# Optimization experiments

Measured on AMD Instinct MI355X. Metric: run time of the kernel, lower is better.

## Reference

```python
import jax, jax.numpy as jnp
import numpy as np

M = 2048          # num_anchors
K = 32            # neighbors_per_anchor
RADIUS = 0.2      # search_radius
EPS = 1e-5        # BatchNorm eps


def _fps(coords, m):
    """Furthest point sampling. coords: [B,N,3] -> idx [B,m] (starts at index 0, as in torch FPS)."""
    B, N, _ = coords.shape

    def step(carry, _):
        dmin, last = carry
        pt = jnp.take_along_axis(coords, last[:, None, None], axis=1)          # [B,1,3]
        d = jnp.sum((coords - pt) ** 2, axis=-1)                                # [B,N]
        dmin = jnp.minimum(dmin, d)
        nxt = jnp.argmax(dmin, axis=-1).astype(jnp.int32)
        return (dmin, nxt), last

    dmin0 = jnp.full((B, N), 1e10, coords.dtype)
    last0 = jnp.zeros((B,), jnp.int32)
    _, idx = jax.lax.scan(step, (dmin0, last0), None, length=m)                 # [m,B]
    return jnp.transpose(idx)                                                   # [B,m]


def _ball_query(radius, k, coords, anchors):
    """First-k points within radius of each anchor; pad with first hit (PointNet++ semantics)."""
    B, N, _ = coords.shape
    d2 = jnp.sum((anchors[:, :, None, :] - coords[:, None, :, :]) ** 2, axis=-1)  # [B,M,N]
    ar = jnp.arange(N, dtype=jnp.int32)
    masked = jnp.where(d2 < radius * radius, ar[None, None, :], N)               # invalid -> N
    neg_top, _ = jax.lax.top_k(-masked, k)                                       # k smallest indices
    nb = -neg_top                                                                # [B,M,K] ascending
    first = nb[..., :1]                                                          # anchor itself always hits
    return jnp.where(nb == N, first, nb)


def _mlp_layer(x, W, g, b):
    """1x1 conv (no bias) + BatchNorm (training-mode batch stats, biased var) + ReLU.
    x: [B,M,K,Cin], W: [Cout,Cin] -> [B,M,K,Cout]."""
    y = jnp.einsum('bmkc,oc->bmko', x, W)
    mu = y.mean(axis=(0, 1, 2))
    var = y.var(axis=(0, 1, 2))
    y = (y - mu) * jax.lax.rsqrt(var + EPS) * g + b
    return jax.nn.relu(y)


def setup_inputs() -> dict:
    key = jax.random.key(0)
    ks = jax.random.split(key, 6)
    B, N, D = 4, 8192, 16
    dims = [D + 3, 64, 64, 128]
    coords = jax.random.uniform(ks[0], (B, N, 3), dtype=jnp.float32)
    features = jax.random.normal(ks[1], (B, N, D), dtype=jnp.float32)
    inp = {'coords': coords, 'features': features}
    for i in range(3):
        inp[f'W{i}'] = jax.random.normal(ks[2 + i], (dims[i + 1], dims[i]), dtype=jnp.float32) * 0.05
        inp[f'g{i}'] = jnp.ones((dims[i + 1],), jnp.float32)
        inp[f'b{i}'] = jnp.zeros((dims[i + 1],), jnp.float32)
    return inp


def reference(coords, features, W0, g0, b0, W1, g1, b1, W2, g2, b2):
    B = coords.shape[0]
    aidx = _fps(coords, M)                                                       # [B,M]
    anchors = jnp.take_along_axis(coords, aidx[..., None], axis=1)               # [B,M,3]
    nb = _ball_query(RADIUS, K, coords, anchors)                                 # [B,M,K]
    bidx = jnp.arange(B)[:, None, None]
    grouped_xyz = coords[bidx, nb] - anchors[:, :, None, :]                      # [B,M,K,3]
    grouped_feats = features[bidx, nb]                                           # [B,M,K,D]
    x = jnp.concatenate([grouped_xyz, grouped_feats], axis=-1)                   # [B,M,K,3+D]
    x = _mlp_layer(x, W0, g0, b0)
    x = _mlp_layer(x, W1, g1, b1)
    x = _mlp_layer(x, W2, g2, b2)
    aggregated = jnp.transpose(x.max(axis=2), (0, 2, 1))                         # [B,C,M]
    return anchors, aggregated
```

## Files before the change

### kernel.cpp

```cpp
#include <hip/hip_runtime.h>

#define BB 4
#define NN 8192
#define MM 2048
#define KK 32
#define RROWS (BB*MM*KK)

__device__ __forceinline__ float dist2(float ax,float ay,float az,float bx,float by,float bz){
    float dx=__fsub_rn(ax,bx), dy=__fsub_rn(ay,by), dz=__fsub_rn(az,bz);
    return __fadd_rn(__fadd_rn(__fmul_rn(dx,dx),__fmul_rn(dy,dy)),__fmul_rn(dz,dz));
}

__global__ __launch_bounds__(512, 2) void fps_kernel(const float* __restrict__ coords,
                                                     float* __restrict__ anchors)
{
    const int b = blockIdx.x, tid = threadIdx.x;
    const float* cb = coords + (size_t)b*NN*3;
    float* ab = anchors + (size_t)b*MM*3;
    float px[16],py[16],pz[16],dmin[16];
#pragma unroll
    for(int j=0;j<16;++j){
        int idx = j*512 + tid;
        px[j]=cb[idx*3+0]; py[j]=cb[idx*3+1]; pz[j]=cb[idx*3+2];
        dmin[j]=1e10f;
    }
    __shared__ unsigned long long slot[2][8];
    const int w = tid>>6;
    float lx=cb[0], ly=cb[1], lz=cb[2];
    if(tid==0){ ab[0]=lx; ab[1]=ly; ab[2]=lz; }
    for(int s=1;s<MM;++s){
        float bv=-1.f; int bi=0;
#pragma unroll
        for(int j=0;j<16;++j){
            float d = dist2(px[j],py[j],pz[j],lx,ly,lz);
            dmin[j]=fminf(dmin[j],d);
            if(dmin[j]>bv){ bv=dmin[j]; bi=j*512+tid; }
        }
        unsigned long long p = ((unsigned long long)__float_as_uint(bv)<<32) | (unsigned)(NN-1-bi);
#pragma unroll
        for(int off=32;off;off>>=1){
            unsigned long long q = __shfl_xor(p, off);
            if(q>p) p=q;
        }
        const int par = s&1;
        if((tid&63)==0) slot[par][w]=p;
        __syncthreads();
        unsigned long long p0=slot[par][0], p1=slot[par][1], p2=slot[par][2], p3=slot[par][3];
        unsigned long long p4=slot[par][4], p5=slot[par][5], p6=slot[par][6], p7=slot[par][7];
        if(p1>p0) p0=p1;
        if(p3>p2) p2=p3;
        if(p5>p4) p4=p5;
        if(p7>p6) p6=p7;
        if(p2>p0) p0=p2;
        if(p6>p4) p4=p6;
        if(p4>p0) p0=p4;
        const int win = NN-1-(int)(unsigned)p0;
        lx=cb[win*3+0]; ly=cb[win*3+1]; lz=cb[win*3+2];
        if(tid==0){ ab[s*3+0]=lx; ab[s*3+1]=ly; ab[s*3+2]=lz; }
    }
}

__global__ __launch_bounds__(256) void ballq_kernel(const float* __restrict__ coords,
                                                    const float* __restrict__ anchors,
                                                    int* __restrict__ nb)
{
    const int wid = threadIdx.x>>6, lane = threadIdx.x&63;
    const int a = blockIdx.x*4 + wid;
    const int b = a >> 11;
    const float* cb = coords + (size_t)b*NN*3;
    const float ax=anchors[a*3+0], ay=anchors[a*3+1], az=anchors[a*3+2];
    const float R2 = (float)(0.2*0.2);
    int* out = nb + (size_t)a*KK;
    int cnt = 0, first = 0;
    for(int base=0; base<NN; base+=64){
        int i = base + lane;
        float d2 = dist2(ax,ay,az, cb[i*3+0],cb[i*3+1],cb[i*3+2]);
        bool in = d2 < R2;
        unsigned long long mask = __ballot(in);
        if(cnt==0 && mask) first = base + (int)__builtin_ctzll(mask);
        int pre = __popcll(mask & ((1ull<<lane)-1ull));
        if(in && (cnt+pre)<KK) out[cnt+pre] = i;
        cnt += __popcll(mask);
        if(cnt>=KK) break;
    }
    if(cnt<KK && lane>=cnt && lane<KK) out[lane] = first;
}

__global__ __launch_bounds__(256) void l0_stats_kernel(
    const float* __restrict__ coords, const float* __restrict__ feats,
    const float* __restrict__ anchors, const int* __restrict__ nb,
    const float* __restrict__ W0, float* __restrict__ stats)
{
    const int r = blockIdx.x*256 + threadIdx.x;
    const int b = r>>16, mk = r&65535, m = mk>>5;
    const int p = nb[r];
    const float* pc = coords + ((size_t)b*NN + p)*3;
    const float* pa = anchors + ((size_t)b*MM + m)*3;
    const float* pf = feats + ((size_t)b*NN + p)*16;
    float x[19];
    x[0]=pc[0]-pa[0]; x[1]=pc[1]-pa[1]; x[2]=pc[2]-pa[2];
#pragma unroll
    for(int c=0;c<16;++c) x[3+c]=pf[c];
    __shared__ float lsum[4][64], lsq[4][64];
    const int lane = threadIdx.x&63, wid = threadIdx.x>>6;
    for(int o=0;o<64;++o){
        const float* w = W0 + o*19;
        float acc=0.f;
#pragma unroll
        for(int c=0;c<19;++c) acc = fmaf(x[c], w[c], acc);
        float s1=acc, s2=acc*acc;
#pragma unroll
        for(int off=32;off>0;off>>=1){ s1+=__shfl_xor(s1,off); s2+=__shfl_xor(s2,off); }
        if(lane==0){ lsum[wid][o]=s1; lsq[wid][o]=s2; }
    }
    __syncthreads();
    if(threadIdx.x<64){
        int o=threadIdx.x;
        atomicAdd(&stats[o],    lsum[0][o]+lsum[1][o]+lsum[2][o]+lsum[3][o]);
        atomicAdd(&stats[64+o], lsq[0][o]+lsq[1][o]+lsq[2][o]+lsq[3][o]);
    }
}

__global__ void fin_kernel(const float* __restrict__ acc, const float* __restrict__ g,
                           const float* __restrict__ bias, float* __restrict__ s,
                           float* __restrict__ sh, int C)
{
    int o = threadIdx.x; if(o>=C) return;
    const float R = (float)RROWS;
    float mu = acc[o]/R;
    float var = acc[C+o]/R - mu*mu;
    if(var<0.f) var=0.f;
    float sc = g[o] * (1.0f/sqrtf(var+1e-5f));
    s[o]=sc; sh[o]=bias[o]-mu*sc;
}

__global__ __launch_bounds__(256) void l1_kernel(
    const float* __restrict__ coords, const float* __restrict__ feats,
    const float* __restrict__ anchors, const int* __restrict__ nb,
    const float* __restrict__ W0, const float* __restrict__ W1,
    const float* __restrict__ s0, const float* __restrict__ sh0,
    float* __restrict__ y1, float* __restrict__ stats)
{
    const int r = blockIdx.x*256 + threadIdx.x;
    const int b = r>>16, mk = r&65535, m = mk>>5;
    const int p = nb[r];
    const float* pc = coords + ((size_t)b*NN + p)*3;
    const float* pa = anchors + ((size_t)b*MM + m)*3;
    const float* pf = feats + ((size_t)b*NN + p)*16;
    float x[19];
    x[0]=pc[0]-pa[0]; x[1]=pc[1]-pa[1]; x[2]=pc[2]-pa[2];
#pragma unroll
    for(int c=0;c<16;++c) x[3+c]=pf[c];
    float x1[64];
#pragma unroll
    for(int o=0;o<64;++o){
        const float* w = W0 + o*19;
        float acc=0.f;
#pragma unroll
        for(int c=0;c<19;++c) acc = fmaf(x[c], w[c], acc);
        x1[o] = fmaxf(fmaf(acc, s0[o], sh0[o]), 0.f);
    }
    __shared__ float lsum[4][64], lsq[4][64];
    const int lane = threadIdx.x&63, wid = threadIdx.x>>6;
    for(int o=0;o<64;++o){
        const float* w = W1 + o*64;
        float acc=0.f;
#pragma unroll
        for(int c=0;c<64;++c) acc = fmaf(x1[c], w[c], acc);
        y1[(size_t)o*RROWS + r] = acc;
        float s1=acc, s2=acc*acc;
#pragma unroll
        for(int off=32;off>0;off>>=1){ s1+=__shfl_xor(s1,off); s2+=__shfl_xor(s2,off); }
        if(lane==0){ lsum[wid][o]=s1; lsq[wid][o]=s2; }
    }
    __syncthreads();
    if(threadIdx.x<64){
        int o=threadIdx.x;
        atomicAdd(&stats[128+o], lsum[0][o]+lsum[1][o]+lsum[2][o]+lsum[3][o]);
        atomicAdd(&stats[192+o], lsq[0][o]+lsq[1][o]+lsq[2][o]+lsq[3][o]);
    }
}

__global__ __launch_bounds__(256) void l2_kernel(
    const float* __restrict__ y1, const float* __restrict__ W2,
    const float* __restrict__ s1, const float* __restrict__ sh1,
    float* __restrict__ maxv, float* __restrict__ minv, float* __restrict__ stats)
{
    const int r = blockIdx.x*256 + threadIdx.x;
    float x1[64];
#pragma unroll
    for(int c=0;c<64;++c)
        x1[c] = fmaxf(fmaf(y1[(size_t)c*RROWS + r], s1[c], sh1[c]), 0.f);
    __shared__ float lsum[4][128], lsq[4][128];
    const int lane = threadIdx.x&63, wid = threadIdx.x>>6;
    const size_t g = (size_t)(r>>5);
    for(int o=0;o<128;++o){
        const float* w = W2 + o*64;
        float acc=0.f;
#pragma unroll
        for(int c=0;c<64;++c) acc = fmaf(x1[c], w[c], acc);
        float mx=acc, mn=acc;
#pragma unroll
        for(int off=16;off>0;off>>=1){ mx=fmaxf(mx,__shfl_xor(mx,off)); mn=fminf(mn,__shfl_xor(mn,off)); }
        float s1v=acc, s2v=acc*acc;
#pragma unroll
        for(int off=32;off>0;off>>=1){ s1v+=__shfl_xor(s1v,off); s2v+=__shfl_xor(s2v,off); }
        if((lane&31)==0){ maxv[g*128+o]=mx; minv[g*128+o]=mn; }
        if(lane==0){ lsum[wid][o]=s1v; lsq[wid][o]=s2v; }
    }
    __syncthreads();
    if(threadIdx.x<128){
        int o=threadIdx.x;
        atomicAdd(&stats[256+o], lsum[0][o]+lsum[1][o]+lsum[2][o]+lsum[3][o]);
        atomicAdd(&stats[384+o], lsq[0][o]+lsq[1][o]+lsq[2][o]+lsq[3][o]);
    }
}

__global__ __launch_bounds__(128) void out_kernel(
    const float* __restrict__ maxv, const float* __restrict__ minv,
    const float* __restrict__ s2, const float* __restrict__ sh2,
    float* __restrict__ agg)
{
    const int gg = blockIdx.x;
    const int o = threadIdx.x;
    float s = s2[o], sh = sh2[o];
    float pick = (s >= 0.f) ? maxv[(size_t)gg*128+o] : minv[(size_t)gg*128+o];
    float v = fmaxf(fmaf(pick, s, sh), 0.f);
    const int b = gg>>11, m = gg&2047;
    agg[((size_t)b*128 + o)*MM + m] = v;
}

extern "C" void kernel_launch(void* const* d_in, const int* in_sizes, int n_in,
                              void* d_out, int out_size, void* d_ws, size_t ws_size,
                              hipStream_t stream) {
    (void)in_sizes; (void)n_in; (void)out_size; (void)ws_size;
    const float* coords = (const float*)d_in[0];
    const float* feats  = (const float*)d_in[1];
    const float* W0 = (const float*)d_in[2];
    const float* g0 = (const float*)d_in[3];
    const float* b0 = (const float*)d_in[4];
    const float* W1 = (const float*)d_in[5];
    const float* g1 = (const float*)d_in[6];
    const float* b1 = (const float*)d_in[7];
    const float* W2 = (const float*)d_in[8];
    const float* g2 = (const float*)d_in[9];
    const float* b2 = (const float*)d_in[10];

    float* out = (float*)d_out;
    float* anchors = out;
    float* agg = out + (size_t)BB*MM*3;

    char* ws = (char*)d_ws;
    int*   nb    = (int*)ws;
    float* y1v   = (float*)(ws + 1048576);
    float* maxv  = (float*)(ws + 1048576 + 67108864);
    float* minv  = maxv + (size_t)BB*MM*128;
    float* stats = minv + (size_t)BB*MM*128;
    float* s0 = stats + 512; float* sh0 = s0 + 64;
    float* s1 = sh0 + 64;    float* sh1 = s1 + 64;
    float* s2 = sh1 + 64;    float* sh2 = s2 + 128;

    hipMemsetAsync(stats, 0, 512*sizeof(float), stream);
    fps_kernel  <<<BB, 512, 0, stream>>>(coords, anchors);
    ballq_kernel<<<BB*MM/4, 256, 0, stream>>>(coords, anchors, nb);
    l0_stats_kernel<<<RROWS/256, 256, 0, stream>>>(coords, feats, anchors, nb, W0, stats);
    fin_kernel  <<<1, 64, 0, stream>>>(stats, g0, b0, s0, sh0, 64);
    l1_kernel   <<<RROWS/256, 256, 0, stream>>>(coords, feats, anchors, nb, W0, W1, s0, sh0, y1v, stats);
    fin_kernel  <<<1, 64, 0, stream>>>(stats+128, g1, b1, s1, sh1, 64);
    l2_kernel   <<<RROWS/256, 256, 0, stream>>>(y1v, W2, s1, sh1, maxv, minv, stats);
    fin_kernel  <<<1, 128, 0, stream>>>(stats+256, g2, b2, s2, sh2, 128);
    out_kernel  <<<BB*MM, 128, 0, stream>>>(maxv, minv, s2, sh2, agg);
}
```

Measured before the change: 2.795 ms.

## Bucket FPS points into spatial cells in LDS and skip unaffected cells

The furthest-point-sampling kernel counting-sorts the points into an 8x8x8 grid held in shared memory. Each cell keeps a bounding radius and its current max min-distance, and each iteration recomputes distances only for cells the new anchor could improve, using a triangle-inequality threshold. This cuts per-iteration distance work and global loads, but adds ballot-driven divergent loops, heavy shared-memory traffic and a large LDS footprint that limits occupancy. Tie-breaking on the original index is kept through packed keys.

```diff
diff --git a/kernel.cpp b/kernel.cpp
--- a/kernel.cpp
+++ b/kernel.cpp
@@ -15,47 +15,139 @@
                                                      float* __restrict__ anchors)
 {
     const int b = blockIdx.x, tid = threadIdx.x;
+    const int lane = tid & 63, w = tid >> 6;
     const float* cb = coords + (size_t)b*NN*3;
     float* ab = anchors + (size_t)b*MM*3;
-    float px[16],py[16],pz[16],dmin[16];
-#pragma unroll
+
+    __shared__ float sx[NN], sy[NN], sz[NN];
+    __shared__ float sdmin[NN];
+    __shared__ unsigned short sidx[NN];
+    __shared__ unsigned int hist[512];
+    __shared__ unsigned long long cellres[512];
+    __shared__ unsigned long long slot[2][8];
+
+    hist[tid] = 0u;
+    __syncthreads();
     for(int j=0;j<16;++j){
-        int idx = j*512 + tid;
-        px[j]=cb[idx*3+0]; py[j]=cb[idx*3+1]; pz[j]=cb[idx*3+2];
-        dmin[j]=1e10f;
-    }
-    __shared__ unsigned long long slot[2][8];
-    const int w = tid>>6;
+        int p = tid*16+j;
+        float x=cb[p*3+0], y=cb[p*3+1], z=cb[p*3+2];
+        int kx=(int)(x*8.f); kx = kx>7?7:kx;
+        int ky=(int)(y*8.f); ky = ky>7?7:ky;
+        int kz=(int)(z*8.f); kz = kz>7?7:kz;
+        atomicAdd(&hist[(kx<<6)|(ky<<3)|kz], 1u);
+    }
+    __syncthreads();
+    if(w==0){
+        unsigned v[8], sum=0u;
+#pragma unroll
+        for(int k=0;k<8;++k) v[k]=hist[lane*8+k];
+#pragma unroll
+        for(int k=0;k<8;++k){ unsigned t=v[k]; v[k]=sum; sum+=t; }
+        unsigned run = sum;
+#pragma unroll
+        for(int d=1;d<64;d<<=1){ unsigned q=__shfl_up(run,d); if(lane>=d) run+=q; }
+        unsigned base = run - sum;
+#pragma unroll
+        for(int k=0;k<8;++k) hist[lane*8+k] = base + v[k];
+    }
+    __syncthreads();
+    for(int j=0;j<16;++j){
+        int p = tid*16+j;
+        float x=cb[p*3+0], y=cb[p*3+1], z=cb[p*3+2];
+        int kx=(int)(x*8.f); kx = kx>7?7:kx;
+        int ky=(int)(y*8.f); ky = ky>7?7:ky;
+        int kz=(int)(z*8.f); kz = kz>7?7:kz;
+        unsigned pos = atomicAdd(&hist[(kx<<6)|(ky<<3)|kz], 1u);
+        sx[pos]=x; sy[pos]=y; sz[pos]=z; sidx[pos]=(unsigned short)p;
+    }
+    __syncthreads();
+    float mnx=1e30f,mny=1e30f,mnz=1e30f,mxx=-1e30f,mxy=-1e30f,mxz=-1e30f;
+#pragma unroll
+    for(int j=0;j<16;++j){
+        int p=tid*16+j;
+        float x=sx[p], y=sy[p], z=sz[p];
+        mnx=fminf(mnx,x); mxx=fmaxf(mxx,x);
+        mny=fminf(mny,y); mxy=fmaxf(mxy,y);
+        mnz=fminf(mnz,z); mxz=fmaxf(mxz,z);
+        sdmin[p]=1e10f;
+    }
+    float ccx=0.5f*(mnx+mxx), ccy=0.5f*(mny+mxy), ccz=0.5f*(mnz+mxz);
+    float r2m=0.f;
+    unsigned bestlow=0u;
+#pragma unroll
+    for(int j=0;j<16;++j){
+        int p=tid*16+j;
+        float dx=sx[p]-ccx, dy=sy[p]-ccy, dz=sz[p]-ccz;
+        float d2c=dx*dx+dy*dy+dz*dz;
+        r2m = fmaxf(r2m, d2c);
+        unsigned lowj = (((unsigned)(8191 - (int)sidx[p]))<<13) | (unsigned)p;
+        bestlow = (lowj>bestlow)?lowj:bestlow;
+    }
+    const float rr = sqrtf(r2m)*1.0001f + 1e-9f;
+    float cmax = 1e10f;
+    unsigned long long cand = ((unsigned long long)__float_as_uint(1e10f)<<32) | bestlow;
+    float cthr = 3.0e38f;
     float lx=cb[0], ly=cb[1], lz=cb[2];
     if(tid==0){ ab[0]=lx; ab[1]=ly; ab[2]=lz; }
+    __syncthreads();
+
     for(int s=1;s<MM;++s){
-        float bv=-1.f; int bi=0;
-#pragma unroll
-        for(int j=0;j<16;++j){
-            float d = dist2(px[j],py[j],pz[j],lx,ly,lz);
-            dmin[j]=fminf(dmin[j],d);
-            if(dmin[j]>bv){ bv=dmin[j]; bi=j*512+tid; }
+        float tdx=ccx-lx, tdy=ccy-ly, tdz=ccz-lz;
+        float t2 = tdx*tdx+tdy*tdy+tdz*tdz;
+        bool kept = t2 < cthr;
+        unsigned long long mask = __ballot(kept);
+        while(mask){
+            int c0=(int)__builtin_ctzll(mask); mask &= mask-1ull;
+            int c1=c0,c2=c0,c3=c0;
+            if(mask){ c1=(int)__builtin_ctzll(mask); mask &= mask-1ull; }
+            if(mask){ c2=(int)__builtin_ctzll(mask); mask &= mask-1ull; }
+            if(mask){ c3=(int)__builtin_ctzll(mask); mask &= mask-1ull; }
+            int g = lane>>4;
+            int cc = (g==0)?c0:((g==1)?c1:((g==2)?c2:c3));
+            int p = ((w<<6)+cc)*16 + (lane&15);
+            float x=sx[p], y=sy[p], z=sz[p];
+            float dm=sdmin[p];
+            float d = dist2(x,y,z,lx,ly,lz);
+            float nd = fminf(dm,d);
+            sdmin[p]=nd;
+            unsigned oi = sidx[p];
+            unsigned long long pkt = ((unsigned long long)__float_as_uint(nd)<<32)
+                                   | (((unsigned)(8191u-oi))<<13) | (unsigned)p;
+#pragma unroll
+            for(int off=1; off<16; off<<=1){
+                unsigned long long q = __shfl_xor(pkt, off);
+                if(q>pkt) pkt=q;
+            }
+            if((lane&15)==0) cellres[(w<<6)+cc] = pkt;
         }
-        unsigned long long p = ((unsigned long long)__float_as_uint(bv)<<32) | (unsigned)(NN-1-bi);
-#pragma unroll
-        for(int off=32;off;off>>=1){
-            unsigned long long q = __shfl_xor(p, off);
-            if(q>p) p=q;
+        asm volatile("s_waitcnt lgkmcnt(0)" ::: "memory");
+        if(kept){
+            unsigned long long pkt = cellres[tid];
+            cand = pkt;
+            cmax = __uint_as_float((unsigned)(pkt>>32));
+            float q = rr + sqrtf(cmax);
+            cthr = q*q*1.0002f;
         }
+        float v = cmax;
+#pragma unroll
+        for(int off=1;off<64;off<<=1) v = fmaxf(v, __shfl_xor(v,off));
+        unsigned lowm = (cmax==v) ? (unsigned)cand : 0u;
+#pragma unroll
+        for(int off=1;off<64;off<<=1){ unsigned q=__shfl_xor(lowm,off); lowm = (q>lowm)?q:lowm; }
         const int par = s&1;
-        if((tid&63)==0) slot[par][w]=p;
+        if(lane==0) slot[par][w] = ((unsigned long long)__float_as_uint(v)<<32) | lowm;
         __syncthreads();
-        unsigned long long p0=slot[par][0], p1=slot[par][1], p2=slot[par][2], p3=slot[par][3];
-        unsigned long long p4=slot[par][4], p5=slot[par][5], p6=slot[par][6], p7=slot[par][7];
-        if(p1>p0) p0=p1;
-        if(p3>p2) p2=p3;
-        if(p5>p4) p4=p5;
-        if(p7>p6) p6=p7;
-        if(p2>p0) p0=p2;
-        if(p6>p4) p4=p6;
-        if(p4>p0) p0=p4;
-        const int win = NN-1-(int)(unsigned)p0;
-        lx=cb[win*3+0]; ly=cb[win*3+1]; lz=cb[win*3+2];
+        unsigned long long p0=slot[par][0],p1=slot[par][1],p2=slot[par][2],p3=slot[par][3];
+        unsigned long long p4=slot[par][4],p5=slot[par][5],p6=slot[par][6],p7=slot[par][7];
+        if(p1>p0)p0=p1;
+        if(p3>p2)p2=p3;
+        if(p5>p4)p4=p5;
+        if(p7>p6)p6=p7;
+        if(p2>p0)p0=p2;
+        if(p6>p4)p4=p6;
+        if(p4>p0)p0=p4;
+        int pos = (int)((unsigned)p0 & 0x1FFFu);
+        lx=sx[pos]; ly=sy[pos]; lz=sz[pos];
         if(tid==0){ ab[s*3+0]=lx; ab[s*3+1]=ly; ab[s*3+2]=lz; }
     }
 }
```

New measurement: 4.675 ms. 67.2% more time.
